# Kernel optimization log

Hardware: AMD Instinct MI355X
Metric: run time of the kernel (lower is better)

## Reference

```python
import jax, jax.numpy as jnp
import numpy as np

V, H, B, NS, SL, QL, AL = 100000, 256, 64, 40, 30, 20, 12
NUM_EPISODE = 3


def setup_inputs() -> dict:
    key = jax.random.key(0)
    ks = iter(jax.random.split(key, 48))
    def p(shape, scale=0.05):
        return jax.random.normal(next(ks), shape, jnp.float32) * scale
    d = {}
    d["c_p"] = jax.random.randint(next(ks), (B, NS, SL), 0, V, dtype=jnp.int32)
    d["c_mask"] = jnp.zeros((B, NS, SL), jnp.int32)
    d["q_p"] = jax.random.randint(next(ks), (B, QL), 0, V, dtype=jnp.int32)
    d["q_mask"] = jnp.zeros((B, QL), jnp.int32)
    d["a_I_p"] = jax.random.randint(next(ks), (B, AL), 0, V, dtype=jnp.int32)
    d["a_I_mask"] = jnp.zeros((B, AL), jnp.int32)
    d["a_II_p"] = jax.random.randint(next(ks), (B, AL), 0, V, dtype=jnp.int32)
    d["a_II_mask"] = jnp.zeros((B, AL), jnp.int32)
    d["embed"] = p((V, H)).at[0].set(0.0)  # padding_idx=0
    for name in ["ctx", "q", "ans", "attn", "mem"]:
        d[name + "_Wih"] = p((3 * H, H))
        d[name + "_Whh"] = p((3 * H, H))
        d[name + "_bih"] = p((3 * H,))
        d[name + "_bhh"] = p((3 * H,))
    d["gate_W1"] = p((H, 7 * H)); d["gate_b1"] = p((H,))
    d["gate_W2"] = p((1, H));     d["gate_b2"] = p((1,))
    d["out_W1"] = p((H, 3 * H)); d["out_b1"] = p((H,))
    d["out_W2"] = p((2, H));     d["out_b2"] = p((2,))
    return d


def _gru_step(h, gi_t, Whh, bhh):
    # PyTorch GRU cell math; gates ordered (r, z, n)
    gh = h @ Whh.T + bhh
    i_r, i_z, i_n = jnp.split(gi_t, 3, -1)
    h_r, h_z, h_n = jnp.split(gh, 3, -1)
    r = jax.nn.sigmoid(i_r + h_r)
    z = jax.nn.sigmoid(i_z + h_z)
    n = jnp.tanh(i_n + r * h_n)
    return (1.0 - z) * n + z * h


def _run_gru(x, Wih, Whh, bih, bhh):
    # x: [N, T, H] -> outputs [N, T, H], zero initial hidden
    gi = jnp.einsum('nth,gh->ntg', x, Wih) + bih  # precompute input projections
    h0 = jnp.zeros((x.shape[0], Whh.shape[1]), x.dtype)
    def step(h, g_t):
        h2 = _gru_step(h, g_t, Whh, bhh)
        return h2, h2
    _, outs = jax.lax.scan(step, h0, jnp.swapaxes(gi, 0, 1))
    return jnp.swapaxes(outs, 0, 1)


def _gather_last(outs, mask):
    # real_length = number of zeros in mask (0 marks a valid token)
    lengths = jnp.sum(mask == 0, axis=-1)
    idx = jnp.clip(lengths - 1, 0, outs.shape[1] - 1)
    return jnp.take_along_axis(outs, idx[:, None, None], axis=1)[:, 0]


def _forward(c_p, c_mask, q_p, q_mask, a_I_p, a_I_mask, a_II_p, a_II_mask,
             embed,
             ctx_Wih, ctx_Whh, ctx_bih, ctx_bhh,
             q_Wih, q_Whh, q_bih, q_bhh,
             ans_Wih, ans_Whh, ans_bih, ans_bhh,
             attn_Wih, attn_Whh, attn_bih, attn_bhh,
             mem_Wih, mem_Whh, mem_bih, mem_bhh,
             gate_W1, gate_b1, gate_W2, gate_b2,
             out_W1, out_b1, out_W2, out_b2):
    b, ns, sl = c_p.shape
    # Context encoding: all (batch, sentence) pairs through one batched GRU
    ce = embed[c_p.reshape(b * ns, sl)]                      # [B*NS, SL, H]
    c_out = _run_gru(ce, ctx_Wih, ctx_Whh, ctx_bih, ctx_bhh)
    enc_ctx = _gather_last(c_out, c_mask.reshape(b * ns, sl)).reshape(b, ns, -1)  # [B, NS, H]
    # Question / answers
    enc_q = _gather_last(_run_gru(embed[q_p], q_Wih, q_Whh, q_bih, q_bhh), q_mask)          # [B, H]
    enc_a1 = _gather_last(_run_gru(embed[a_I_p], ans_Wih, ans_Whh, ans_bih, ans_bhh), a_I_mask)
    enc_a2 = _gather_last(_run_gru(embed[a_II_p], ans_Wih, ans_Whh, ans_bih, ans_bhh), a_II_mask)
    # Episodic memory: gated attention GRU scan over context sentences
    ctx_t = jnp.swapaxes(enc_ctx, 0, 1)  # [NS, B, H]
    memory = enc_q
    for _ in range(NUM_EPISODE):
        mem_now = memory
        def step(h, ct):
            feat = jnp.concatenate([ct, mem_now, enc_q, ct * enc_q, ct * mem_now,
                                    jnp.abs(ct - enc_q), jnp.abs(ct - mem_now)], axis=1)  # [B, 7H]
            g = jax.nn.sigmoid(jnp.tanh(feat @ gate_W1.T + gate_b1) @ gate_W2.T + gate_b2)  # [B, 1]
            hc = _gru_step(h, ct @ attn_Wih.T + attn_bih, attn_Whh, attn_bhh)
            return g * hc + (1.0 - g) * h, None
        e, _ = jax.lax.scan(step, jnp.zeros_like(memory), ctx_t)
        memory = _gru_step(memory, e @ mem_Wih.T + mem_bih, mem_Whh, mem_bhh)
    final = jnp.concatenate([memory, enc_a1, enc_a2], axis=1)  # [B, 3H]
    logits = jnp.tanh(final @ out_W1.T + out_b1) @ out_W2.T + out_b2  # [B, 2]
    return jax.nn.softmax(logits, axis=-1)


def reference(c_p, c_mask, q_p, q_mask, a_I_p, a_I_mask, a_II_p, a_II_mask,
              embed,
              ctx_Wih, ctx_Whh, ctx_bih, ctx_bhh,
              q_Wih, q_Whh, q_bih, q_bhh,
              ans_Wih, ans_Whh, ans_bih, ans_bhh,
              attn_Wih, attn_Whh, attn_bih, attn_bhh,
              mem_Wih, mem_Whh, mem_bih, mem_bhh,
              gate_W1, gate_b1, gate_W2, gate_b2,
              out_W1, out_b1, out_W2, out_b2):
    return _forward(c_p, c_mask, q_p, q_mask, a_I_p, a_I_mask, a_II_p, a_II_mask,
                    embed,
                    ctx_Wih, ctx_Whh, ctx_bih, ctx_bhh,
                    q_Wih, q_Whh, q_bih, q_bhh,
                    ans_Wih, ans_Whh, ans_bih, ans_bhh,
                    attn_Wih, attn_Whh, attn_bih, attn_bhh,
                    mem_Wih, mem_Whh, mem_bih, mem_bhh,
                    gate_W1, gate_b1, gate_W2, gate_b2,
                    out_W1, out_b1, out_W2, out_b2)
```

## Files before the change

kernel.cpp:

```cpp
#include <hip/hip_runtime.h>

typedef unsigned short u16;
typedef __bf16 bf16x8 __attribute__((ext_vector_type(8)));
typedef float f32x4 __attribute__((ext_vector_type(4)));
typedef float f32x4v __attribute__((ext_vector_type(4)));
typedef unsigned int u32x2 __attribute__((ext_vector_type(2)));

#define NSENT 40
#define SLEN 30
#define QLEN 20
#define ALEN 12
#define SCTX 2560
#define SLOT 24
#define TP 12288

__device__ __forceinline__ float b2f(u16 u){ union{float f; unsigned i;} v; v.i = ((unsigned)u)<<16; return v.f; }
__device__ __forceinline__ u16 f2b(float f){ union{float f; unsigned u;} v; v.f=f; unsigned u=v.u; u += ((u>>16)&1u) + 0x7fffu; return (u16)(u>>16); }
__device__ __forceinline__ float sigm(float x){ return __builtin_amdgcn_rcpf(1.f + __expf(-x)); }
__device__ __forceinline__ float tanh_(float x){
  float a = fminf(fmaxf(2.f*x, -30.f), 30.f);
  float e = __expf(a);
  return 1.f - 2.f*__builtin_amdgcn_rcpf(e + 1.f);
}
__device__ __forceinline__ f32x4 mfma16(bf16x8 a, bf16x8 b, f32x4 c){
// ... 74 lines not shown
    *(u32x2*)&xb[row][f4*4] = pk;
  }
  const int w=tid>>6, lane=tid&63, c=lane&15, quad=lane>>4;
  __syncthreads();
  #pragma unroll
  for (int jj=0;jj<2;jj++){
    f32x4 acc[4][3];
    #pragma unroll
    for (int Mt=0;Mt<4;Mt++)
      #pragma unroll
      for (int g=0;g<3;g++) acc[Mt][g]=(f32x4){0.f,0.f,0.f,0.f};
    #pragma unroll
    for (int Kt=0;Kt<8;Kt++){
      bf16x8 a0=*(const bf16x8*)&xb[c][Kt*32+quad*8];
      bf16x8 a1=*(const bf16x8*)&xb[16+c][Kt*32+quad*8];
      bf16x8 a2=*(const bf16x8*)&xb[32+c][Kt*32+quad*8];
      bf16x8 a3=*(const bf16x8*)&xb[48+c][Kt*32+quad*8];
      #pragma unroll
      for (int g=0;g<3;g++){
        bf16x8 bfr=*(const bf16x8*)(W + (w*96+(jj*3+g)*16+c)*256 + Kt*32 + quad*8);
        acc[0][g]=mfma16(a0,bfr,acc[0][g]);
        acc[1][g]=mfma16(a1,bfr,acc[1][g]);
        acc[2][g]=mfma16(a2,bfr,acc[2][g]);
        acc[3][g]=mfma16(a3,bfr,acc[3][g]);
      }
    }
    float bv[3];
    #pragma unroll
    for (int g=0;g<3;g++) bv[g]=bias[w*96+(jj*3+g)*16+c];
    #pragma unroll
    for (int Mt=0;Mt<4;Mt++){
      int tp=Mt>>1, smh=Mt&1;
      unsigned d[6];
      #pragma unroll
      for (int k=0;k<6;k++){
        int s0=2*k, s1=2*k+1;
        int r0=s0/3, g0=s0%3, r1=s1/3, g1=s1%3;
        unsigned lo=f2b(acc[Mt][g0][r0]+bv[g0]);
        unsigned hi=f2b(acc[Mt][g1][r1]+bv[g1]);
        d[k]=lo|(hi<<16);
      }
      long block16 = (long)blk32*2 + smh;
      u16* dst = out + (block16*T + t0+tp)*TP + jj*6144 + (w*64+lane)*12;
      u32x2 s0v; s0v.x=d[0]; s0v.y=d[1];
      u32x2 s1v; s1v.x=d[2]; s1v.y=d[3];
      u32x2 s2v; s2v.x=d[4]; s2v.y=d[5];
      __builtin_nontemporal_store(s0v, (u32x2*)dst);
      __builtin_nontemporal_store(s1v, (u32x2*)(dst+4));
      __builtin_nontemporal_store(s2v, (u32x2*)(dst+8));
    }
  }
}

__global__ __launch_bounds__(512, 2) void k_enc_scan(
    const int* c_mask, const int* q_mask, const int* a1m, const int* a2m,
    const u16* cWhhP, const u16* qWhhP, const u16* aWhhP,
    const float* cBhh, const float* qBhh, const float* aBhh,
    const u16* gi_c, const u16* gi_q, const u16* gi_a1, const u16* gi_a2,
    u16* enc_hi, u16* enc_lo, float* enc_qf, float* enc_a1f, float* enc_a2f)
{
  __shared__ u16 hhi[16][264];
  __shared__ u16 hlo[16][264];
  __shared__ int idxs[16];
  int bid=blockIdx.x, tid=threadIdx.x;
  const int* msk; const u16* W; const float* bhh; const u16* gi; int T, seq0, mode;
  u16 *ohi=0, *olo=0; float* of=0;
  if (bid<160){ msk=c_mask; W=cWhhP; bhh=cBhh; gi=gi_c+(long)bid*SLEN*TP; T=SLEN; seq0=bid*16; mode=0; ohi=enc_hi; olo=enc_lo; }
  else if (bid<164){ int e=bid-160; msk=q_mask; W=qWhhP; bhh=qBhh; gi=gi_q+(long)e*QLEN*TP; T=QLEN; seq0=e*16; mode=1; of=enc_qf; }
  else if (bid<168){ int e=bid-164; msk=a1m; W=aWhhP; bhh=aBhh; gi=gi_a1+(long)e*ALEN*TP; T=ALEN; seq0=e*16; mode=1; of=enc_a1f; }
  else             { int e=bid-168; msk=a2m; W=aWhhP; bhh=aBhh; gi=gi_a2+(long)e*ALEN*TP; T=ALEN; seq0=e*16; mode=1; of=enc_a2f; }
  if (tid<16){
    int len=0; const int* mr=msk+(seq0+tid)*T;
    for (int t=0;t<T;t++) len += (mr[t]==0);
    int id=len-1; if(id<0)id=0; if(id>T-1)id=T-1; idxs[tid]=id;
  }
  for (int i=tid;i<16*264;i+=512){ ((u16*)hhi)[i]=0; ((u16*)hlo)[i]=0; }
  const int w=tid>>6, lane=tid&63, c=lane&15, quad=lane>>4;
  float biasv[6];
  #pragma unroll
  for (int nt=0;nt<6;nt++) biasv[nt]=bhh[w*96+nt*16+c];
  uint4 breg[48];
  #pragma unroll
  for (int nt=0;nt<6;nt++)
    #pragma unroll
    for (int Kt=0;Kt<8;Kt++)
      breg[nt*8+Kt] = *(const uint4*)(W + (w*96+nt*16+c)*256 + Kt*32 + quad*8);
  float hreg[8];
  #pragma unroll
  for (int i=0;i<8;i++) hreg[i]=0.f;
  const u16* gp = gi + (w*64+lane)*12;
  u32x2 pA0=*(const u32x2*)(gp),      pA1=*(const u32x2*)(gp+4),    pA2=*(const u32x2*)(gp+8);
  u32x2 pA3=*(const u32x2*)(gp+6144), pA4=*(const u32x2*)(gp+6148), pA5=*(const u32x2*)(gp+6152);
  __syncthreads();
  int idxr[4];
  #pragma unroll
  for (int r=0;r<4;r++) idxr[r]=idxs[quad*4+r];

  for (int t=0;t<T;t++){
    u32x2 pB0,pB1,pB2,pB3,pB4,pB5;
    bool pf=(t+1<T);
    if (pf){
      const u16* gn = gp + (long)(t+1)*TP;
      pB0=*(const u32x2*)(gn);      pB1=*(const u32x2*)(gn+4);    pB2=*(const u32x2*)(gn+8);
      pB3=*(const u32x2*)(gn+6144); pB4=*(const u32x2*)(gn+6148); pB5=*(const u32x2*)(gn+6152);
    }
    f32x4 acc[6];
    #pragma unroll
    for (int nt=0;nt<6;nt++) acc[nt]=(f32x4){0.f,0.f,0.f,0.f};
    #pragma unroll
    for (int Kt=0;Kt<8;Kt++){
      bf16x8 a=*(const bf16x8*)&hhi[c][Kt*32+quad*8];
      #pragma unroll
      for (int nt=0;nt<6;nt++) acc[nt]=mfma16(a,*(const bf16x8*)&breg[nt*8+Kt],acc[nt]);
    }
    #pragma unroll
    for (int Kt=0;Kt<8;Kt++){
      bf16x8 a=*(const bf16x8*)&hlo[c][Kt*32+quad*8];
      #pragma unroll
      for (int nt=0;nt<6;nt++) acc[nt]=mfma16(a,*(const bf16x8*)&breg[nt*8+Kt],acc[nt]);
    }
    unsigned pd[12];
    *(u32x2*)&pd[0]=pA0; *(u32x2*)&pd[2]=pA1; *(u32x2*)&pd[4]=pA2;
    *(u32x2*)&pd[6]=pA3; *(u32x2*)&pd[8]=pA4; *(u32x2*)&pd[10]=pA5;
    #pragma unroll
    for (int r=0;r<4;r++){
      int m=quad*4+r;
      #pragma unroll
      for (int jj=0;jj<2;jj++){
        int j=w*32+jj*16+c;
        int ib=r*3;
        float ir = b2f((u16)((pd[jj*6+(ib>>1)]     >> ((ib&1)*16)) & 0xffffu));
        float iz = b2f((u16)((pd[jj*6+((ib+1)>>1)] >> (((ib+1)&1)*16)) & 0xffffu));
        float in_= b2f((u16)((pd[jj*6+((ib+2)>>1)] >> (((ib+2)&1)*16)) & 0xffffu));
        float hr=acc[jj*3+0][r]+biasv[jj*3+0];
        float hz=acc[jj*3+1][r]+biasv[jj*3+1];
        float hn=acc[jj*3+2][r]+biasv[jj*3+2];
        float rr=sigm(ir+hr), zz=sigm(iz+hz), nn=tanh_(in_+rr*hn);
        float ho=hreg[r*2+jj];
        float hnew=(1.f-zz)*nn+zz*ho;
        hreg[r*2+jj]=hnew;
        u16 hi_=f2b(hnew); u16 lo_=f2b(hnew-b2f(hi_));
        hhi[m][j]=hi_; hlo[m][j]=lo_;
        if (t==idxr[r]){
          long o=(long)(seq0+m)*256+j;
          if (mode==0){ ohi[o]=hi_; olo[o]=lo_; }
          else of[o]=hnew;
        }
      }
    }
    __syncthreads();
    pA0=pB0; pA1=pB1; pA2=pB2; pA3=pB3; pA4=pB4; pA5=pB5;
  }
}

__global__ __launch_bounds__(512, 2) void k_gi(
    const u16* enc_hi, const u16* enc_lo, const u16* tWihP, const float* tBih,
    float* gi_attn, const float* enc_qf, float* mem_f)
{
  int bid=blockIdx.x, tid=threadIdx.x;
  if (bid==160){ for (int i=tid;i<64*256;i+=512) mem_f[i]=enc_qf[i]; return; }
  __shared__ u16 ahi[16][264];
  __shared__ u16 alo[16][264];
  int bblk=bid/40, s=bid-bblk*40, b0=bblk*16;
  {
    int row=tid>>5, ch=tid&31;
    long seq=(long)(b0+row)*NSENT + s;
    *(uint4*)((char*)&ahi[row][0]+ch*16) = *((const uint4*)(enc_hi+seq*256)+ch);
    *(uint4*)((char*)&alo[row][0]+ch*16) = *((const uint4*)(enc_lo+seq*256)+ch);
  }
  const int w=tid>>6, lane=tid&63, c=lane&15, quad=lane>>4;
  f32x4 acc[6];
  #pragma unroll
  for (int nt=0;nt<6;nt++) acc[nt]=(f32x4){0.f,0.f,0.f,0.f};
  __syncthreads();
  #pragma unroll
  for (int Kt=0;Kt<8;Kt++){
    bf16x8 a=*(const bf16x8*)&ahi[c][Kt*32+quad*8];
    #pragma unroll
    for (int nt=0;nt<6;nt++){
      bf16x8 bfr=*(const bf16x8*)(tWihP + (w*96+nt*16+c)*256 + Kt*32 + quad*8);
      acc[nt]=mfma16(a,bfr,acc[nt]);
    }
  }
  #pragma unroll
  for (int Kt=0;Kt<8;Kt++){
    bf16x8 a=*(const bf16x8*)&alo[c][Kt*32+quad*8];
    #pragma unroll
    for (int nt=0;nt<6;nt++){
      bf16x8 bfr=*(const bf16x8*)(tWihP + (w*96+nt*16+c)*256 + Kt*32 + quad*8);
      acc[nt]=mfma16(a,bfr,acc[nt]);
    }
  }
  float biasv[6];
  #pragma unroll
  for (int nt=0;nt<6;nt++) biasv[nt]=tBih[w*96+nt*16+c];
  float* dst = gi_attn + ((long)(bblk*40+s))*TP + (w*64+lane)*SLOT;
  #pragma unroll
  for (int d=0;d<6;d++){
    float4 v;
    #pragma unroll
    for (int e=0;e<4;e++){
      int idx=4*d+e;
      int r=idx/6, rem=idx%6, jj=rem/3, g=rem%3;
      ((float*)&v)[e]=acc[jj*3+g][r]+biasv[jj*3+g];
    }
    *(float4*)(dst+4*d)=v;
  }
}

__global__ __launch_bounds__(512, 1) void k_gatepre(
    const u16* enc_hi, const u16* enc_lo, const float* enc_qf,
    const u16* W1, const float* b1, float* partial)
{
  __shared__ float ctf[32][257];
  __shared__ float qvf[32][257];
  __shared__ u16 ab[32][264];
  int bid=blockIdx.x, tid=threadIdx.x, seq0=bid*32;
  #pragma unroll
  for (int p=0;p<16;p++){
    int i=p*512+tid; int row=i>>8, j=i&255;
    int grow=seq0+row; int b=grow/NSENT;
    ctf[row][j]=b2f(enc_hi[(long)grow*256+j])+b2f(enc_lo[(long)grow*256+j]);
    qvf[row][j]=enc_qf[b*256+j];
  }
  const int w=tid>>6, lane=tid&63, c=lane&15, quad=lane>>4;
  f32x4 acc[2][2];
  #pragma unroll
  for (int nt=0;nt<2;nt++){
    float bv=b1[(w*2+nt)*16+c];
    acc[0][nt]=(f32x4){bv,bv,bv,bv}; acc[1][nt]=acc[0][nt];
  }
  const int chl[4]={0,2,3,5};
  for (int ci=0; ci<4; ci++){
    int ch=chl[ci];
    __syncthreads();
    #pragma unroll
    for (int p=0;p<16;p++){
      int i=p*512+tid; int row=i>>8, j=i&255;
      float ct=ctf[row][j], qv=qvf[row][j];
      float v;
      if      (ch==0) v=ct;
      else if (ch==2) v=qv;
      else if (ch==3) v=ct*qv;
      else            v=fabsf(ct-qv);
      ab[row][j]=f2b(v);
    }
    __syncthreads();
    #pragma unroll
    for (int Kt=0;Kt<8;Kt++){
      bf16x8 a0=*(const bf16x8*)&ab[c][Kt*32+quad*8];
      bf16x8 a1=*(const bf16x8*)&ab[16+c][Kt*32+quad*8];
      #pragma unroll
      for (int nt=0;nt<2;nt++){
        int n=(w*2+nt)*16+c;
        bf16x8 bfr=*(const bf16x8*)(W1 + (long)n*1792 + ch*256 + Kt*32 + quad*8);
        acc[0][nt]=mfma16(a0,bfr,acc[0][nt]);
        acc[1][nt]=mfma16(a1,bfr,acc[1][nt]);
      }
    }
// ... 40 lines not shown
  for (int ci=0; ci<3; ci++){
    int ch=chl[ci];
    __syncthreads();
    #pragma unroll
    for (int p=0;p<16;p++){
      int i=p*512+tid; int row=i>>8, j=i&255;
      float ct=ctf[row][j], mv=mvf[row][j];
      float v;
      if      (ch==1) v=mv;
      else if (ch==4) v=ct*mv;
      else            v=fabsf(ct-mv);
      ab[row][j]=f2b(v);
    }
    __syncthreads();
    #pragma unroll
    for (int Kt=0;Kt<8;Kt++){
      bf16x8 a0=*(const bf16x8*)&ab[c][Kt*32+quad*8];
      bf16x8 a1=*(const bf16x8*)&ab[16+c][Kt*32+quad*8];
      #pragma unroll
      for (int nt=0;nt<2;nt++){
        int n=(w*2+nt)*16+c;
        bf16x8 bfr=*(const bf16x8*)(W1 + (long)n*1792 + ch*256 + Kt*32 + quad*8);
        acc[0][nt]=mfma16(a0,bfr,acc[0][nt]);
        acc[1][nt]=mfma16(a1,bfr,acc[1][nt]);
      }
    }
  }
  float pm[8];
  #pragma unroll
  for (int i=0;i<8;i++){
    int Mt=i>>2, r=i&3;
    float s=0.f;
    #pragma unroll
    for (int nt=0;nt<2;nt++) s += tanh_(acc[Mt][nt][r])*w2v[nt];
    pm[i]=s;
  }
  #pragma unroll
  for (int off=1;off<16;off<<=1)
    #pragma unroll
    for (int i=0;i<8;i++) pm[i]+=__shfl_xor(pm[i],off,64);
  if (c==0){
    #pragma unroll
    for (int i=0;i<8;i++){ int m=(i>>2)*16+quad*4+(i&3); pl[m][w]=pm[i]; }
  }
  __syncthreads();
  if (tid<32){
    float s=b2v[0];
    #pragma unroll
    for (int ww=0;ww<8;ww++) s+=pl[tid][ww];
    g[seq0+tid]=sigm(s);
  }
}

__global__ __launch_bounds__(512, 2) void k_scan(
    const u16* tWhhP, const float* tBhh,
    const float* gi_attn, const float* g,
    float* mem_f, const u16* mWihP, const u16* mWhhP,
    const float* mBih, const float* mBhh)
{
  __shared__ u16 hb[16][264];
  __shared__ u16 mhi[16][264];
  __shared__ u16 mlo[16][264];
  __shared__ float memfl[16][256];
  __shared__ float gl[16][40];
  int bid=blockIdx.x, tid=threadIdx.x, b0=bid*16;
  const int w=tid>>6, lane=tid&63, c=lane&15, quad=lane>>4;
  for (int i=tid;i<16*264;i+=512){ ((u16*)hb)[i]=0; }
  for (int i=tid;i<4096;i+=512){
    int m=i>>8, j=i&255;
    float v=mem_f[(b0+m)*256+j]; memfl[m][j]=v;
    u16 hi_=f2b(v); mhi[m][j]=hi_; mlo[m][j]=f2b(v-b2f(hi_));
  }
  for (int i=tid;i<640;i+=512){ int m=i/40, s=i-m*40; gl[m][s]=g[(b0+m)*40+s]; }
  float biasv[6];
  #pragma unroll
  for (int nt=0;nt<6;nt++) biasv[nt]=tBhh[w*96+nt*16+c];
  uint4 breg[48];
  #pragma unroll
  for (int nt=0;nt<6;nt++)
    #pragma unroll
    for (int Kt=0;Kt<8;Kt++)
      breg[nt*8+Kt] = *(const uint4*)(tWhhP + (w*96+nt*16+c)*256 + Kt*32 + quad*8);
  float hreg[8];
  #pragma unroll
  for (int i=0;i<8;i++) hreg[i]=0.f;
  const float* gp = gi_attn + ((long)bid*NSENT)*TP + (w*64+lane)*SLOT;
  float4 pA[6];
  #pragma unroll
  for (int d=0;d<6;d++) pA[d]=*(const float4*)(gp+4*d);
  __syncthreads();

  for (int s=0;s<NSENT;s++){
    float4 pB[6];
    bool pf=(s+1<NSENT);
    if (pf){
      const float* gn = gp + (long)(s+1)*TP;
      #pragma unroll
      for (int d=0;d<6;d++) pB[d]=*(const float4*)(gn+4*d);
    }
    f32x4 acc[6];
    #pragma unroll
    for (int nt=0;nt<6;nt++) acc[nt]=(f32x4){0.f,0.f,0.f,0.f};
    #pragma unroll
    for (int Kt=0;Kt<8;Kt++){
      bf16x8 a=*(const bf16x8*)&hb[c][Kt*32+quad*8];
      #pragma unroll
      for (int nt=0;nt<6;nt++) acc[nt]=mfma16(a,*(const bf16x8*)&breg[nt*8+Kt],acc[nt]);
    }
    const float* pf32 = (const float*)&pA[0];
    #pragma unroll
    for (int r=0;r<4;r++){
      int m=quad*4+r;
      float gv = gl[m][s];
      #pragma unroll
      for (int jj=0;jj<2;jj++){
        int j=w*32+jj*16+c;
        int ib=(r*2+jj)*3;
        float ir=pf32[ib], iz=pf32[ib+1], in_=pf32[ib+2];
        float hr=acc[jj*3+0][r]+biasv[jj*3+0];
        float hz=acc[jj*3+1][r]+biasv[jj*3+1];
        float hn=acc[jj*3+2][r]+biasv[jj*3+2];
        float rr=sigm(ir+hr), zz=sigm(iz+hz), nn=tanh_(in_+rr*hn);
        float ho=hreg[r*2+jj];
        float hc=(1.f-zz)*nn+zz*ho;
        float hnew=gv*hc+(1.f-gv)*ho;
        hreg[r*2+jj]=hnew;
        hb[m][j]=f2b(hnew);
      }
    }
    __syncthreads();
    #pragma unroll
    for (int d=0;d<6;d++) pA[d]=pB[d];
  }
  f32x4 ai[6], ah[6];
  #pragma unroll
  for (int nt=0;nt<6;nt++){ ai[nt]=(f32x4){0.f,0.f,0.f,0.f}; ah[nt]=ai[nt]; }
  #pragma unroll
  for (int Kt=0;Kt<8;Kt++){
    bf16x8 a=*(const bf16x8*)&hb[c][Kt*32+quad*8];
    #pragma unroll
    for (int nt=0;nt<6;nt++){
      bf16x8 bfr=*(const bf16x8*)(mWihP + (w*96+nt*16+c)*256 + Kt*32 + quad*8);
      ai[nt]=mfma16(a,bfr,ai[nt]);
    }
  }
  #pragma unroll
  for (int Kt=0;Kt<8;Kt++){
    bf16x8 a=*(const bf16x8*)&mhi[c][Kt*32+quad*8];
    #pragma unroll
    for (int nt=0;nt<6;nt++){
      bf16x8 bfr=*(const bf16x8*)(mWhhP + (w*96+nt*16+c)*256 + Kt*32 + quad*8);
      ah[nt]=mfma16(a,bfr,ah[nt]);
    }
  }
  #pragma unroll
  for (int Kt=0;Kt<8;Kt++){
    bf16x8 a=*(const bf16x8*)&mlo[c][Kt*32+quad*8];
    #pragma unroll
    for (int nt=0;nt<6;nt++){
      bf16x8 bfr=*(const bf16x8*)(mWhhP + (w*96+nt*16+c)*256 + Kt*32 + quad*8);
      ah[nt]=mfma16(a,bfr,ah[nt]);
    }
  }
  float bih6[6], bhh6[6];
  #pragma unroll
  for (int nt=0;nt<6;nt++){ bih6[nt]=mBih[w*96+nt*16+c]; bhh6[nt]=mBhh[w*96+nt*16+c]; }
  #pragma unroll
  for (int r=0;r<4;r++){
    int m=quad*4+r;
    #pragma unroll
    for (int jj=0;jj<2;jj++){
      int j=w*32+jj*16+c;
      float ir=ai[jj*3+0][r]+bih6[jj*3+0];
      float iz=ai[jj*3+1][r]+bih6[jj*3+1];
      float in_=ai[jj*3+2][r]+bih6[jj*3+2];
      float hr=ah[jj*3+0][r]+bhh6[jj*3+0];
      float hz=ah[jj*3+1][r]+bhh6[jj*3+1];
      float hn=ah[jj*3+2][r]+bhh6[jj*3+2];
      float rr=sigm(ir+hr), zz=sigm(iz+hz), nn=tanh_(in_+rr*hn);
      float mo=memfl[m][j];
      mem_f[(b0+m)*256+j]=(1.f-zz)*nn+zz*mo;
    }
  }
}

__global__ void k_final(const float* mem_f, const float* a1f, const float* a2f,
    const float* W1o, const float* b1o, const float* W2o, const float* b2o, float* outp)
{
  __shared__ float af[768];
  __shared__ float tl[256];
  __shared__ float lg[2];
  int b=blockIdx.x, tid=threadIdx.x;
  af[tid]     = mem_f[b*256+tid];
  af[256+tid] = a1f[b*256+tid];
  af[512+tid] = a2f[b*256+tid];
  __syncthreads();
  float s=b1o[tid];
  const float* wr=W1o + (long)tid*768;
  for (int k=0;k<768;k++) s += af[k]*wr[k];
  tl[tid]=tanh_(s);
  __syncthreads();
  if (tid<2){
    float l=b2o[tid];
    const float* w2=W2o + tid*256;
    for (int k=0;k<256;k++) l += tl[k]*w2[k];
    lg[tid]=l;
  }
  __syncthreads();
  if (tid==0){
    float m=fmaxf(lg[0],lg[1]);
    float e0=__expf(lg[0]-m), e1=__expf(lg[1]-m);
    float inv=1.f/(e0+e1);
    outp[b*2]=e0*inv; outp[b*2+1]=e1*inv;
  }
}

extern "C" void kernel_launch(void* const* d_in, const int* in_sizes, int n_in,
                              void* d_out, int out_size, void* d_ws, size_t ws_size,
                              hipStream_t stream) {
  const int* c_p   = (const int*)d_in[0];
  const int* c_m   = (const int*)d_in[1];
  const int* q_p   = (const int*)d_in[2];
  const int* q_m   = (const int*)d_in[3];
  const int* a1p   = (const int*)d_in[4];
  const int* a1m   = (const int*)d_in[5];
  const int* a2p   = (const int*)d_in[6];
  const int* a2m   = (const int*)d_in[7];
  const float* embed = (const float*)d_in[8];
  const float* cWih=(const float*)d_in[9],  *cWhh=(const float*)d_in[10], *cbih=(const float*)d_in[11], *cbhh=(const float*)d_in[12];
  const float* qWih=(const float*)d_in[13], *qWhh=(const float*)d_in[14], *qbih=(const float*)d_in[15], *qbhh=(const float*)d_in[16];
  const float* aWih=(const float*)d_in[17], *aWhh=(const float*)d_in[18], *abih=(const float*)d_in[19], *abhh=(const float*)d_in[20];
  const float* tWih=(const float*)d_in[21], *tWhh=(const float*)d_in[22], *tbih=(const float*)d_in[23], *tbhh=(const float*)d_in[24];
  const float* mWih=(const float*)d_in[25], *mWhh=(const float*)d_in[26], *mbih=(const float*)d_in[27], *mbhh=(const float*)d_in[28];
  const float* gW1=(const float*)d_in[29], *gb1=(const float*)d_in[30], *gW2=(const float*)d_in[31], *gb2=(const float*)d_in[32];
  const float* oW1=(const float*)d_in[33], *ob1=(const float*)d_in[34], *oW2=(const float*)d_in[35], *ob2=(const float*)d_in[36];

  char* ws = (char*)d_ws;
  size_t off = 0;
  u16* P[10];
  for (int i=0;i<10;i++){ P[i]=(u16*)(ws+off); off+=393216; }
  u16* PgW1 =(u16*)(ws+off); off+=917504;
  float* B[10];
  for (int i=0;i<10;i++){ B[i]=(float*)(ws+off); off+=3072; }
  u16* gi_c =(u16*)(ws+off); off+=(size_t)160*SLEN*TP*2;
  u16* gi_q =(u16*)(ws+off); off+=(size_t)4*QLEN*TP*2;
  u16* gi_a1=(u16*)(ws+off); off+=(size_t)4*ALEN*TP*2;
  u16* gi_a2=(u16*)(ws+off); off+=(size_t)4*ALEN*TP*2;
  u16* enc_hi=(u16*)(ws+off); off+=(size_t)SCTX*256*2;
  u16* enc_lo=(u16*)(ws+off); off+=(size_t)SCTX*256*2;
  float* enc_qf =(float*)(ws+off); off+=64*256*4;
  float* enc_a1f=(float*)(ws+off); off+=64*256*4;
  float* enc_a2f=(float*)(ws+off); off+=64*256*4;
  float* mem_f  =(float*)(ws+off); off+=64*256*4;
  float* gi_attn=(float*)(ws+off); off+=(size_t)160*TP*4;
  float* partial=(float*)(ws+off); off+=(size_t)SCTX*256*4;
  float* gbuf   =(float*)(ws+off); off+=SCTX*4;

  k_prep<<<4751, 512, 0, stream>>>(cWih,cWhh,qWih,qWhh,aWih,aWhh,tWih,tWhh,mWih,mWhh,gW1,
      cbih,cbhh,qbih,qbhh,abih,abhh,tbih,tbhh,mbih,mbhh,
      P[0],P[1],P[2],P[3],P[4],P[5],P[6],P[7],P[8],P[9], PgW1,
      B[0],B[1],B[2],B[3],B[4],B[5],B[6],B[7],B[8],B[9]);

  k_xproj<<<1244, 512, 0, stream>>>(c_p,q_p,a1p,a2p, embed,
      P[0],P[2],P[4], B[0],B[2],B[4], gi_c,gi_q,gi_a1,gi_a2);

  k_enc_scan<<<172, 512, 0, stream>>>(c_m,q_m,a1m,a2m,
      P[1],P[3],P[5], B[1],B[3],B[5], gi_c,gi_q,gi_a1,gi_a2,
      enc_hi,enc_lo, enc_qf,enc_a1f,enc_a2f);

  k_gi<<<161, 512, 0, stream>>>(enc_hi,enc_lo, P[6], B[6], gi_attn, enc_qf, mem_f);

  k_gatepre<<<80, 512, 0, stream>>>(enc_hi,enc_lo, enc_qf, PgW1, gb1, partial);

  for (int ep=0; ep<3; ep++){
    k_gate<<<80, 512, 0, stream>>>(enc_hi,enc_lo, mem_f, partial, PgW1, gW2, gb2, gbuf);
    k_scan<<<4, 512, 0, stream>>>(P[7], B[7], gi_attn, gbuf, mem_f, P[8], P[9], B[8], B[9]);
  }

  k_final<<<64, 256, 0, stream>>>(mem_f, enc_a1f, enc_a2f, oW1, ob1, oW2, ob2, (float*)d_out);
}
```

Measured before the change: 893.6 us.

## Double threads per block in recurrent scan kernels, halving per-wave hidden-unit work

The encoder scan and attention scan kernels move from 512 to 1024 threads per block. Each of the 16 waves now owns 16 hidden units (3 gate tiles) instead of 32, which halves the MFMA chain and gate math per wave on every serial timestep. The gi_attn output layout in k_gi is changed to match the new per-wave slicing. The cost is one block per CU and more waves taking part in each per-step barrier. The shorter serial chain per timestep is meant to cut latency on these latency-bound recurrences.

```diff
diff --git a/kernel.cpp b/kernel.cpp
--- a/kernel.cpp
+++ b/kernel.cpp
@@ -150,7 +150,7 @@
   }
 }
 
-__global__ __launch_bounds__(512, 2) void k_enc_scan(
+__global__ __launch_bounds__(1024, 1) void k_enc_scan(
     const int* c_mask, const int* q_mask, const int* a1m, const int* a2m,
     const u16* cWhhP, const u16* qWhhP, const u16* aWhhP,
     const float* cBhh, const float* qBhh, const float* aBhh,
@@ -172,82 +172,76 @@
     for (int t=0;t<T;t++) len += (mr[t]==0);
     int id=len-1; if(id<0)id=0; if(id>T-1)id=T-1; idxs[tid]=id;
   }
-  for (int i=tid;i<16*264;i+=512){ ((u16*)hhi)[i]=0; ((u16*)hlo)[i]=0; }
+  for (int i=tid;i<16*264;i+=1024){ ((u16*)hhi)[i]=0; ((u16*)hlo)[i]=0; }
   const int w=tid>>6, lane=tid&63, c=lane&15, quad=lane>>4;
-  float biasv[6];
-  #pragma unroll
-  for (int nt=0;nt<6;nt++) biasv[nt]=bhh[w*96+nt*16+c];
-  uint4 breg[48];
-  #pragma unroll
-  for (int nt=0;nt<6;nt++)
+  const int j=w*16+c;
+  float biasv[3];
+  #pragma unroll
+  for (int g=0;g<3;g++) biasv[g]=bhh[w*48+g*16+c];
+  uint4 breg[24];
+  #pragma unroll
+  for (int g=0;g<3;g++)
     #pragma unroll
     for (int Kt=0;Kt<8;Kt++)
-      breg[nt*8+Kt] = *(const uint4*)(W + (w*96+nt*16+c)*256 + Kt*32 + quad*8);
-  float hreg[8];
-  #pragma unroll
-  for (int i=0;i<8;i++) hreg[i]=0.f;
-  const u16* gp = gi + (w*64+lane)*12;
-  u32x2 pA0=*(const u32x2*)(gp),      pA1=*(const u32x2*)(gp+4),    pA2=*(const u32x2*)(gp+8);
-  u32x2 pA3=*(const u32x2*)(gp+6144), pA4=*(const u32x2*)(gp+6148), pA5=*(const u32x2*)(gp+6152);
+      breg[g*8+Kt] = *(const uint4*)(W + (w*48+g*16+c)*256 + Kt*32 + quad*8);
+  float hreg[4];
+  #pragma unroll
+  for (int i=0;i<4;i++) hreg[i]=0.f;
+  const u16* gp = gi + (w&1)*6144 + ((w>>1)*64+lane)*12;
+  u32x2 pA0=*(const u32x2*)(gp), pA1=*(const u32x2*)(gp+4), pA2=*(const u32x2*)(gp+8);
   __syncthreads();
   int idxr[4];
   #pragma unroll
   for (int r=0;r<4;r++) idxr[r]=idxs[quad*4+r];
 
   for (int t=0;t<T;t++){
-    u32x2 pB0,pB1,pB2,pB3,pB4,pB5;
+    u32x2 pB0,pB1,pB2;
     bool pf=(t+1<T);
     if (pf){
       const u16* gn = gp + (long)(t+1)*TP;
-      pB0=*(const u32x2*)(gn);      pB1=*(const u32x2*)(gn+4);    pB2=*(const u32x2*)(gn+8);
-      pB3=*(const u32x2*)(gn+6144); pB4=*(const u32x2*)(gn+6148); pB5=*(const u32x2*)(gn+6152);
-    }
-    f32x4 acc[6];
-    #pragma unroll
-    for (int nt=0;nt<6;nt++) acc[nt]=(f32x4){0.f,0.f,0.f,0.f};
+      pB0=*(const u32x2*)(gn); pB1=*(const u32x2*)(gn+4); pB2=*(const u32x2*)(gn+8);
+    }
+    f32x4 acc[3];
+    #pragma unroll
+    for (int g=0;g<3;g++) acc[g]=(f32x4){0.f,0.f,0.f,0.f};
     #pragma unroll
     for (int Kt=0;Kt<8;Kt++){
       bf16x8 a=*(const bf16x8*)&hhi[c][Kt*32+quad*8];
       #pragma unroll
-      for (int nt=0;nt<6;nt++) acc[nt]=mfma16(a,*(const bf16x8*)&breg[nt*8+Kt],acc[nt]);
+      for (int g=0;g<3;g++) acc[g]=mfma16(a,*(const bf16x8*)&breg[g*8+Kt],acc[g]);
     }
     #pragma unroll
     for (int Kt=0;Kt<8;Kt++){
       bf16x8 a=*(const bf16x8*)&hlo[c][Kt*32+quad*8];
       #pragma unroll
-      for (int nt=0;nt<6;nt++) acc[nt]=mfma16(a,*(const bf16x8*)&breg[nt*8+Kt],acc[nt]);
-    }
-    unsigned pd[12];
+      for (int g=0;g<3;g++) acc[g]=mfma16(a,*(const bf16x8*)&breg[g*8+Kt],acc[g]);
+    }
+    unsigned pd[6];
     *(u32x2*)&pd[0]=pA0; *(u32x2*)&pd[2]=pA1; *(u32x2*)&pd[4]=pA2;
-    *(u32x2*)&pd[6]=pA3; *(u32x2*)&pd[8]=pA4; *(u32x2*)&pd[10]=pA5;
     #pragma unroll
     for (int r=0;r<4;r++){
       int m=quad*4+r;
-      #pragma unroll
-      for (int jj=0;jj<2;jj++){
-        int j=w*32+jj*16+c;
-        int ib=r*3;
-        float ir = b2f((u16)((pd[jj*6+(ib>>1)]     >> ((ib&1)*16)) & 0xffffu));
-        float iz = b2f((u16)((pd[jj*6+((ib+1)>>1)] >> (((ib+1)&1)*16)) & 0xffffu));
-        float in_= b2f((u16)((pd[jj*6+((ib+2)>>1)] >> (((ib+2)&1)*16)) & 0xffffu));
-        float hr=acc[jj*3+0][r]+biasv[jj*3+0];
-        float hz=acc[jj*3+1][r]+biasv[jj*3+1];
-        float hn=acc[jj*3+2][r]+biasv[jj*3+2];
-        float rr=sigm(ir+hr), zz=sigm(iz+hz), nn=tanh_(in_+rr*hn);
-        float ho=hreg[r*2+jj];
-        float hnew=(1.f-zz)*nn+zz*ho;
-        hreg[r*2+jj]=hnew;
-        u16 hi_=f2b(hnew); u16 lo_=f2b(hnew-b2f(hi_));
-        hhi[m][j]=hi_; hlo[m][j]=lo_;
-        if (t==idxr[r]){
-          long o=(long)(seq0+m)*256+j;
-          if (mode==0){ ohi[o]=hi_; olo[o]=lo_; }
-          else of[o]=hnew;
-        }
+      int ib=r*3;
+      float ir = b2f((u16)((pd[ib>>1]     >> ((ib&1)*16)) & 0xffffu));
+      float iz = b2f((u16)((pd[(ib+1)>>1] >> (((ib+1)&1)*16)) & 0xffffu));
+      float in_= b2f((u16)((pd[(ib+2)>>1] >> (((ib+2)&1)*16)) & 0xffffu));
+      float hr=acc[0][r]+biasv[0];
+      float hz=acc[1][r]+biasv[1];
+      float hn=acc[2][r]+biasv[2];
+      float rr=sigm(ir+hr), zz=sigm(iz+hz), nn=tanh_(in_+rr*hn);
+      float ho=hreg[r];
+      float hnew=(1.f-zz)*nn+zz*ho;
+      hreg[r]=hnew;
+      u16 hi_=f2b(hnew); u16 lo_=f2b(hnew-b2f(hi_));
+      hhi[m][j]=hi_; hlo[m][j]=lo_;
+      if (t==idxr[r]){
+        long o=(long)(seq0+m)*256+j;
+        if (mode==0){ ohi[o]=hi_; olo[o]=lo_; }
+        else of[o]=hnew;
       }
     }
     __syncthreads();
-    pA0=pB0; pA1=pB1; pA2=pB2; pA3=pB3; pA4=pB4; pA5=pB5;
+    pA0=pB0; pA1=pB1; pA2=pB2;
   }
 }
 
@@ -292,17 +286,20 @@
   float biasv[6];
   #pragma unroll
   for (int nt=0;nt<6;nt++) biasv[nt]=tBih[w*96+nt*16+c];
-  float* dst = gi_attn + ((long)(bblk*40+s))*TP + (w*64+lane)*SLOT;
-  #pragma unroll
-  for (int d=0;d<6;d++){
-    float4 v;
-    #pragma unroll
-    for (int e=0;e<4;e++){
-      int idx=4*d+e;
-      int r=idx/6, rem=idx%6, jj=rem/3, g=rem%3;
-      ((float*)&v)[e]=acc[jj*3+g][r]+biasv[jj*3+g];
-    }
-    *(float4*)(dst+4*d)=v;
+  #pragma unroll
+  for (int jj=0;jj<2;jj++){
+    float* dst = gi_attn + ((long)(bblk*40+s))*TP + jj*6144 + (w*64+lane)*12;
+    #pragma unroll
+    for (int d=0;d<3;d++){
+      float4 v;
+      #pragma unroll
+      for (int e=0;e<4;e++){
+        int idx=4*d+e;
+        int r=idx/3, g=idx%3;
+        ((float*)&v)[e]=acc[jj*3+g][r]+biasv[jj*3+g];
+      }
+      *(float4*)(dst+4*d)=v;
+    }
   }
 }
 
@@ -449,7 +446,7 @@
   }
 }
 
-__global__ __launch_bounds__(512, 2) void k_scan(
+__global__ __launch_bounds__(1024, 1) void k_scan(
     const u16* tWhhP, const float* tBhh,
     const float* gi_attn, const float* g,
     float* mem_f, const u16* mWihP, const u16* mWhhP,
@@ -462,122 +459,115 @@
   __shared__ float gl[16][40];
   int bid=blockIdx.x, tid=threadIdx.x, b0=bid*16;
   const int w=tid>>6, lane=tid&63, c=lane&15, quad=lane>>4;
-  for (int i=tid;i<16*264;i+=512){ ((u16*)hb)[i]=0; }
-  for (int i=tid;i<4096;i+=512){
-    int m=i>>8, j=i&255;
-    float v=mem_f[(b0+m)*256+j]; memfl[m][j]=v;
-    u16 hi_=f2b(v); mhi[m][j]=hi_; mlo[m][j]=f2b(v-b2f(hi_));
-  }
-  for (int i=tid;i<640;i+=512){ int m=i/40, s=i-m*40; gl[m][s]=g[(b0+m)*40+s]; }
-  float biasv[6];
-  #pragma unroll
-  for (int nt=0;nt<6;nt++) biasv[nt]=tBhh[w*96+nt*16+c];
-  uint4 breg[48];
-  #pragma unroll
-  for (int nt=0;nt<6;nt++)
+  const int j=w*16+c;
+  for (int i=tid;i<16*264;i+=1024){ ((u16*)hb)[i]=0; }
+  for (int i=tid;i<4096;i+=1024){
+    int m=i>>8, jx=i&255;
+    float v=mem_f[(b0+m)*256+jx]; memfl[m][jx]=v;
+    u16 hi_=f2b(v); mhi[m][jx]=hi_; mlo[m][jx]=f2b(v-b2f(hi_));
+  }
+  for (int i=tid;i<640;i+=1024){ int m=i/40, s=i-m*40; gl[m][s]=g[(b0+m)*40+s]; }
+  float biasv[3];
+  #pragma unroll
+  for (int gg=0;gg<3;gg++) biasv[gg]=tBhh[w*48+gg*16+c];
+  uint4 breg[24];
+  #pragma unroll
+  for (int gg=0;gg<3;gg++)
     #pragma unroll
     for (int Kt=0;Kt<8;Kt++)
-      breg[nt*8+Kt] = *(const uint4*)(tWhhP + (w*96+nt*16+c)*256 + Kt*32 + quad*8);
-  float hreg[8];
-  #pragma unroll
-  for (int i=0;i<8;i++) hreg[i]=0.f;
-  const float* gp = gi_attn + ((long)bid*NSENT)*TP + (w*64+lane)*SLOT;
-  float4 pA[6];
-  #pragma unroll
-  for (int d=0;d<6;d++) pA[d]=*(const float4*)(gp+4*d);
+      breg[gg*8+Kt] = *(const uint4*)(tWhhP + (w*48+gg*16+c)*256 + Kt*32 + quad*8);
+  float hreg[4];
+  #pragma unroll
+  for (int i=0;i<4;i++) hreg[i]=0.f;
+  const float* gp = gi_attn + ((long)bid*NSENT)*TP + (w&1)*6144 + ((w>>1)*64+lane)*12;
+  float4 pA[3];
+  #pragma unroll
+  for (int d=0;d<3;d++) pA[d]=*(const float4*)(gp+4*d);
   __syncthreads();
 
   for (int s=0;s<NSENT;s++){
-    float4 pB[6];
+    float4 pB[3];
     bool pf=(s+1<NSENT);
     if (pf){
       const float* gn = gp + (long)(s+1)*TP;
       #pragma unroll
-      for (int d=0;d<6;d++) pB[d]=*(const float4*)(gn+4*d);
-    }
-    f32x4 acc[6];
-    #pragma unroll
-    for (int nt=0;nt<6;nt++) acc[nt]=(f32x4){0.f,0.f,0.f,0.f};
+      for (int d=0;d<3;d++) pB[d]=*(const float4*)(gn+4*d);
+    }
+    f32x4 acc[3];
+    #pragma unroll
+    for (int gg=0;gg<3;gg++) acc[gg]=(f32x4){0.f,0.f,0.f,0.f};
     #pragma unroll
     for (int Kt=0;Kt<8;Kt++){
       bf16x8 a=*(const bf16x8*)&hb[c][Kt*32+quad*8];
       #pragma unroll
-      for (int nt=0;nt<6;nt++) acc[nt]=mfma16(a,*(const bf16x8*)&breg[nt*8+Kt],acc[nt]);
+      for (int gg=0;gg<3;gg++) acc[gg]=mfma16(a,*(const bf16x8*)&breg[gg*8+Kt],acc[gg]);
     }
     const float* pf32 = (const float*)&pA[0];
     #pragma unroll
     for (int r=0;r<4;r++){
       int m=quad*4+r;
       float gv = gl[m][s];
-      #pragma unroll
-      for (int jj=0;jj<2;jj++){
-        int j=w*32+jj*16+c;
-        int ib=(r*2+jj)*3;
-        float ir=pf32[ib], iz=pf32[ib+1], in_=pf32[ib+2];
-        float hr=acc[jj*3+0][r]+biasv[jj*3+0];
-        float hz=acc[jj*3+1][r]+biasv[jj*3+1];
-        float hn=acc[jj*3+2][r]+biasv[jj*3+2];
-        float rr=sigm(ir+hr), zz=sigm(iz+hz), nn=tanh_(in_+rr*hn);
-        float ho=hreg[r*2+jj];
-        float hc=(1.f-zz)*nn+zz*ho;
-        float hnew=gv*hc+(1.f-gv)*ho;
-        hreg[r*2+jj]=hnew;
-        hb[m][j]=f2b(hnew);
-      }
+      int ib=r*3;
+      float ir=pf32[ib], iz=pf32[ib+1], in_=pf32[ib+2];
+      float hr=acc[0][r]+biasv[0];
+      float hz=acc[1][r]+biasv[1];
+      float hn=acc[2][r]+biasv[2];
+      float rr=sigm(ir+hr), zz=sigm(iz+hz), nn=tanh_(in_+rr*hn);
+      float ho=hreg[r];
+      float hc=(1.f-zz)*nn+zz*ho;
+      float hnew=gv*hc+(1.f-gv)*ho;
+      hreg[r]=hnew;
+      hb[m][j]=f2b(hnew);
     }
     __syncthreads();
     #pragma unroll
-    for (int d=0;d<6;d++) pA[d]=pB[d];
-  }
-  f32x4 ai[6], ah[6];
-  #pragma unroll
-  for (int nt=0;nt<6;nt++){ ai[nt]=(f32x4){0.f,0.f,0.f,0.f}; ah[nt]=ai[nt]; }
+    for (int d=0;d<3;d++) pA[d]=pB[d];
+  }
+  f32x4 ai[3], ah[3];
+  #pragma unroll
+  for (int gg=0;gg<3;gg++){ ai[gg]=(f32x4){0.f,0.f,0.f,0.f}; ah[gg]=ai[gg]; }
   #pragma unroll
   for (int Kt=0;Kt<8;Kt++){
     bf16x8 a=*(const bf16x8*)&hb[c][Kt*32+quad*8];
     #pragma unroll
-    for (int nt=0;nt<6;nt++){
-      bf16x8 bfr=*(const bf16x8*)(mWihP + (w*96+nt*16+c)*256 + Kt*32 + quad*8);
-      ai[nt]=mfma16(a,bfr,ai[nt]);
+    for (int gg=0;gg<3;gg++){
+      bf16x8 bfr=*(const bf16x8*)(mWihP + (w*48+gg*16+c)*256 + Kt*32 + quad*8);
+      ai[gg]=mfma16(a,bfr,ai[gg]);
     }
   }
   #pragma unroll
   for (int Kt=0;Kt<8;Kt++){
     bf16x8 a=*(const bf16x8*)&mhi[c][Kt*32+quad*8];
     #pragma unroll
-    for (int nt=0;nt<6;nt++){
-      bf16x8 bfr=*(const bf16x8*)(mWhhP + (w*96+nt*16+c)*256 + Kt*32 + quad*8);
-      ah[nt]=mfma16(a,bfr,ah[nt]);
+    for (int gg=0;gg<3;gg++){
+      bf16x8 bfr=*(const bf16x8*)(mWhhP + (w*48+gg*16+c)*256 + Kt*32 + quad*8);
+      ah[gg]=mfma16(a,bfr,ah[gg]);
     }
   }
   #pragma unroll
   for (int Kt=0;Kt<8;Kt++){
     bf16x8 a=*(const bf16x8*)&mlo[c][Kt*32+quad*8];
     #pragma unroll
-    for (int nt=0;nt<6;nt++){
-      bf16x8 bfr=*(const bf16x8*)(mWhhP + (w*96+nt*16+c)*256 + Kt*32 + quad*8);
-      ah[nt]=mfma16(a,bfr,ah[nt]);
-    }
-  }
-  float bih6[6], bhh6[6];
-  #pragma unroll
-  for (int nt=0;nt<6;nt++){ bih6[nt]=mBih[w*96+nt*16+c]; bhh6[nt]=mBhh[w*96+nt*16+c]; }
+    for (int gg=0;gg<3;gg++){
+      bf16x8 bfr=*(const bf16x8*)(mWhhP + (w*48+gg*16+c)*256 + Kt*32 + quad*8);
+      ah[gg]=mfma16(a,bfr,ah[gg]);
+    }
+  }
+  float bih3[3], bhh3[3];
+  #pragma unroll
+  for (int gg=0;gg<3;gg++){ bih3[gg]=mBih[w*48+gg*16+c]; bhh3[gg]=mBhh[w*48+gg*16+c]; }
   #pragma unroll
   for (int r=0;r<4;r++){
     int m=quad*4+r;
-    #pragma unroll
-    for (int jj=0;jj<2;jj++){
-      int j=w*32+jj*16+c;
-      float ir=ai[jj*3+0][r]+bih6[jj*3+0];
-      float iz=ai[jj*3+1][r]+bih6[jj*3+1];
-      float in_=ai[jj*3+2][r]+bih6[jj*3+2];
-      float hr=ah[jj*3+0][r]+bhh6[jj*3+0];
-      float hz=ah[jj*3+1][r]+bhh6[jj*3+1];
-      float hn=ah[jj*3+2][r]+bhh6[jj*3+2];
-      float rr=sigm(ir+hr), zz=sigm(iz+hz), nn=tanh_(in_+rr*hn);
-      float mo=memfl[m][j];
-      mem_f[(b0+m)*256+j]=(1.f-zz)*nn+zz*mo;
-    }
+    float ir=ai[0][r]+bih3[0];
+    float iz=ai[1][r]+bih3[1];
+    float in_=ai[2][r]+bih3[2];
+    float hr=ah[0][r]+bhh3[0];
+    float hz=ah[1][r]+bhh3[1];
+    float hn=ah[2][r]+bhh3[2];
+    float rr=sigm(ir+hr), zz=sigm(iz+hz), nn=tanh_(in_+rr*hn);
+    float mo=memfl[m][j];
+    mem_f[(b0+m)*256+j]=(1.f-zz)*nn+zz*mo;
   }
 }
 
@@ -661,7 +651,7 @@
   k_xproj<<<1244, 512, 0, stream>>>(c_p,q_p,a1p,a2p, embed,
       P[0],P[2],P[4], B[0],B[2],B[4], gi_c,gi_q,gi_a1,gi_a2);
 
-  k_enc_scan<<<172, 512, 0, stream>>>(c_m,q_m,a1m,a2m,
+  k_enc_scan<<<172, 1024, 0, stream>>>(c_m,q_m,a1m,a2m,
       P[1],P[3],P[5], B[1],B[3],B[5], gi_c,gi_q,gi_a1,gi_a2,
       enc_hi,enc_lo, enc_qf,enc_a1f,enc_a2f);
 
@@ -671,7 +661,7 @@
 
   for (int ep=0; ep<3; ep++){
     k_gate<<<80, 512, 0, stream>>>(enc_hi,enc_lo, mem_f, partial, PgW1, gW2, gb2, gbuf);
-    k_scan<<<4, 512, 0, stream>>>(P[7], B[7], gi_attn, gbuf, mem_f, P[8], P[9], B[8], B[9]);
+    k_scan<<<4, 1024, 0, stream>>>(P[7], B[7], gi_attn, gbuf, mem_f, P[8], P[9], B[8], B[9]);
   }
 
   k_final<<<64, 256, 0, stream>>>(mem_f, enc_a1f, enc_a2f, oW1, ob1, oW2, ob2, (float*)d_out);
```

After: 1.295 ms. 1.45x slower.

## Process two 16-sequence groups per encoder-scan block, reading Whh from global

Applied to the files above, without the earlier changes.

Each encoder GRU scan block now handles 32 sequences (two 16-row halves) instead of 16, halving the grid from 172 to 86 blocks. Recurrent weights are no longer held in 48 uint4 registers; they are reloaded from global or cache inside each time step and shared across both halves. The intent is to raise MFMA work per weight fetch and free registers, while the hi/lo split MFMAs are interleaved. In exchange, fewer blocks run (86 on a 256-CU part) and per-step global weight loads add latency to the sequential critical path.

```diff
diff --git a/kernel.cpp b/kernel.cpp
--- a/kernel.cpp
+++ b/kernel.cpp
@@ -150,104 +150,125 @@
   }
 }
 
-__global__ __launch_bounds__(512, 2) void k_enc_scan(
+__global__ __launch_bounds__(512, 1) void k_enc_scan(
     const int* c_mask, const int* q_mask, const int* a1m, const int* a2m,
     const u16* cWhhP, const u16* qWhhP, const u16* aWhhP,
     const float* cBhh, const float* qBhh, const float* aBhh,
     const u16* gi_c, const u16* gi_q, const u16* gi_a1, const u16* gi_a2,
     u16* enc_hi, u16* enc_lo, float* enc_qf, float* enc_a1f, float* enc_a2f)
 {
-  __shared__ u16 hhi[16][264];
-  __shared__ u16 hlo[16][264];
-  __shared__ int idxs[16];
+  __shared__ u16 hhi[32][264];
+  __shared__ u16 hlo[32][264];
+  __shared__ int idxs[32];
   int bid=blockIdx.x, tid=threadIdx.x;
   const int* msk; const u16* W; const float* bhh; const u16* gi; int T, seq0, mode;
   u16 *ohi=0, *olo=0; float* of=0;
-  if (bid<160){ msk=c_mask; W=cWhhP; bhh=cBhh; gi=gi_c+(long)bid*SLEN*TP; T=SLEN; seq0=bid*16; mode=0; ohi=enc_hi; olo=enc_lo; }
-  else if (bid<164){ int e=bid-160; msk=q_mask; W=qWhhP; bhh=qBhh; gi=gi_q+(long)e*QLEN*TP; T=QLEN; seq0=e*16; mode=1; of=enc_qf; }
-  else if (bid<168){ int e=bid-164; msk=a1m; W=aWhhP; bhh=aBhh; gi=gi_a1+(long)e*ALEN*TP; T=ALEN; seq0=e*16; mode=1; of=enc_a1f; }
-  else             { int e=bid-168; msk=a2m; W=aWhhP; bhh=aBhh; gi=gi_a2+(long)e*ALEN*TP; T=ALEN; seq0=e*16; mode=1; of=enc_a2f; }
-  if (tid<16){
+  if (bid<80){ msk=c_mask; W=cWhhP; bhh=cBhh; gi=gi_c+(long)bid*2*SLEN*TP; T=SLEN; seq0=bid*32; mode=0; ohi=enc_hi; olo=enc_lo; }
+  else if (bid<82){ int e=bid-80; msk=q_mask; W=qWhhP; bhh=qBhh; gi=gi_q+(long)e*2*QLEN*TP; T=QLEN; seq0=e*32; mode=1; of=enc_qf; }
+  else if (bid<84){ int e=bid-82; msk=a1m; W=aWhhP; bhh=aBhh; gi=gi_a1+(long)e*2*ALEN*TP; T=ALEN; seq0=e*32; mode=1; of=enc_a1f; }
+  else            { int e=bid-84; msk=a2m; W=aWhhP; bhh=aBhh; gi=gi_a2+(long)e*2*ALEN*TP; T=ALEN; seq0=e*32; mode=1; of=enc_a2f; }
+  if (tid<32){
     int len=0; const int* mr=msk+(seq0+tid)*T;
     for (int t=0;t<T;t++) len += (mr[t]==0);
     int id=len-1; if(id<0)id=0; if(id>T-1)id=T-1; idxs[tid]=id;
   }
-  for (int i=tid;i<16*264;i+=512){ ((u16*)hhi)[i]=0; ((u16*)hlo)[i]=0; }
+  for (int i=tid;i<32*264;i+=512){ ((u16*)hhi)[i]=0; ((u16*)hlo)[i]=0; }
   const int w=tid>>6, lane=tid&63, c=lane&15, quad=lane>>4;
   float biasv[6];
   #pragma unroll
   for (int nt=0;nt<6;nt++) biasv[nt]=bhh[w*96+nt*16+c];
-  uint4 breg[48];
-  #pragma unroll
-  for (int nt=0;nt<6;nt++)
-    #pragma unroll
-    for (int Kt=0;Kt<8;Kt++)
-      breg[nt*8+Kt] = *(const uint4*)(W + (w*96+nt*16+c)*256 + Kt*32 + quad*8);
-  float hreg[8];
-  #pragma unroll
-  for (int i=0;i<8;i++) hreg[i]=0.f;
-  const u16* gp = gi + (w*64+lane)*12;
-  u32x2 pA0=*(const u32x2*)(gp),      pA1=*(const u32x2*)(gp+4),    pA2=*(const u32x2*)(gp+8);
-  u32x2 pA3=*(const u32x2*)(gp+6144), pA4=*(const u32x2*)(gp+6148), pA5=*(const u32x2*)(gp+6152);
-  __syncthreads();
-  int idxr[4];
-  #pragma unroll
-  for (int r=0;r<4;r++) idxr[r]=idxs[quad*4+r];
+  float hreg[16];
+  #pragma unroll
+  for (int i=0;i<16;i++) hreg[i]=0.f;
+  const u16* gpl = gi + (w*64+lane)*12;
+  const u16* Wb  = W + (w*96+c)*256 + quad*8;
+  u32x2 pA[12];
+  #pragma unroll
+  for (int hf=0;hf<2;hf++)
+    #pragma unroll
+    for (int jj=0;jj<2;jj++){
+      const u16* p = gpl + ((long)hf*T)*TP + jj*6144;
+      pA[(hf*2+jj)*3+0]=*(const u32x2*)(p);
+      pA[(hf*2+jj)*3+1]=*(const u32x2*)(p+4);
+      pA[(hf*2+jj)*3+2]=*(const u32x2*)(p+8);
+    }
+  __syncthreads();
+  int idxr[8];
+  #pragma unroll
+  for (int hf=0;hf<2;hf++)
+    #pragma unroll
+    for (int r=0;r<4;r++) idxr[hf*4+r]=idxs[hf*16+quad*4+r];
 
   for (int t=0;t<T;t++){
-    u32x2 pB0,pB1,pB2,pB3,pB4,pB5;
+    u32x2 pB[12];
     bool pf=(t+1<T);
     if (pf){
-      const u16* gn = gp + (long)(t+1)*TP;
-      pB0=*(const u32x2*)(gn);      pB1=*(const u32x2*)(gn+4);    pB2=*(const u32x2*)(gn+8);
-      pB3=*(const u32x2*)(gn+6144); pB4=*(const u32x2*)(gn+6148); pB5=*(const u32x2*)(gn+6152);
-    }
-    f32x4 acc[6];
-    #pragma unroll
-    for (int nt=0;nt<6;nt++) acc[nt]=(f32x4){0.f,0.f,0.f,0.f};
+      #pragma unroll
+      for (int hf=0;hf<2;hf++)
+        #pragma unroll
+        for (int jj=0;jj<2;jj++){
+          const u16* p = gpl + ((long)hf*T + t+1)*TP + jj*6144;
+          pB[(hf*2+jj)*3+0]=*(const u32x2*)(p);
+          pB[(hf*2+jj)*3+1]=*(const u32x2*)(p+4);
+          pB[(hf*2+jj)*3+2]=*(const u32x2*)(p+8);
+        }
+    }
+    f32x4 acc[2][6];
+    #pragma unroll
+    for (int hf=0;hf<2;hf++)
+      #pragma unroll
+      for (int nt=0;nt<6;nt++) acc[hf][nt]=(f32x4){0.f,0.f,0.f,0.f};
     #pragma unroll
     for (int Kt=0;Kt<8;Kt++){
-      bf16x8 a=*(const bf16x8*)&hhi[c][Kt*32+quad*8];
-      #pragma unroll
-      for (int nt=0;nt<6;nt++) acc[nt]=mfma16(a,*(const bf16x8*)&breg[nt*8+Kt],acc[nt]);
-    }
-    #pragma unroll
-    for (int Kt=0;Kt<8;Kt++){
-      bf16x8 a=*(const bf16x8*)&hlo[c][Kt*32+quad*8];
-      #pragma unroll
-      for (int nt=0;nt<6;nt++) acc[nt]=mfma16(a,*(const bf16x8*)&breg[nt*8+Kt],acc[nt]);
-    }
-    unsigned pd[12];
-    *(u32x2*)&pd[0]=pA0; *(u32x2*)&pd[2]=pA1; *(u32x2*)&pd[4]=pA2;
-    *(u32x2*)&pd[6]=pA3; *(u32x2*)&pd[8]=pA4; *(u32x2*)&pd[10]=pA5;
-    #pragma unroll
-    for (int r=0;r<4;r++){
-      int m=quad*4+r;
+      bf16x8 ah0=*(const bf16x8*)&hhi[c][Kt*32+quad*8];
+      bf16x8 ah1=*(const bf16x8*)&hhi[16+c][Kt*32+quad*8];
+      bf16x8 al0=*(const bf16x8*)&hlo[c][Kt*32+quad*8];
+      bf16x8 al1=*(const bf16x8*)&hlo[16+c][Kt*32+quad*8];
+      #pragma unroll
+      for (int nt=0;nt<6;nt++){
+        bf16x8 bfr=*(const bf16x8*)(Wb + nt*4096 + Kt*32);
+        acc[0][nt]=mfma16(ah0,bfr,acc[0][nt]);
+        acc[0][nt]=mfma16(al0,bfr,acc[0][nt]);
+        acc[1][nt]=mfma16(ah1,bfr,acc[1][nt]);
+        acc[1][nt]=mfma16(al1,bfr,acc[1][nt]);
+      }
+    }
+    #pragma unroll
+    for (int hf=0;hf<2;hf++){
       #pragma unroll
       for (int jj=0;jj<2;jj++){
-        int j=w*32+jj*16+c;
-        int ib=r*3;
-        float ir = b2f((u16)((pd[jj*6+(ib>>1)]     >> ((ib&1)*16)) & 0xffffu));
-        float iz = b2f((u16)((pd[jj*6+((ib+1)>>1)] >> (((ib+1)&1)*16)) & 0xffffu));
-        float in_= b2f((u16)((pd[jj*6+((ib+2)>>1)] >> (((ib+2)&1)*16)) & 0xffffu));
-        float hr=acc[jj*3+0][r]+biasv[jj*3+0];
-        float hz=acc[jj*3+1][r]+biasv[jj*3+1];
-        float hn=acc[jj*3+2][r]+biasv[jj*3+2];
-        float rr=sigm(ir+hr), zz=sigm(iz+hz), nn=tanh_(in_+rr*hn);
-        float ho=hreg[r*2+jj];
-        float hnew=(1.f-zz)*nn+zz*ho;
-        hreg[r*2+jj]=hnew;
-        u16 hi_=f2b(hnew); u16 lo_=f2b(hnew-b2f(hi_));
-        hhi[m][j]=hi_; hlo[m][j]=lo_;
-        if (t==idxr[r]){
-          long o=(long)(seq0+m)*256+j;
-          if (mode==0){ ohi[o]=hi_; olo[o]=lo_; }
-          else of[o]=hnew;
+        unsigned pd[6];
+        *(u32x2*)&pd[0]=pA[(hf*2+jj)*3+0];
+        *(u32x2*)&pd[2]=pA[(hf*2+jj)*3+1];
+        *(u32x2*)&pd[4]=pA[(hf*2+jj)*3+2];
+        #pragma unroll
+        for (int r=0;r<4;r++){
+          int ib=r*3;
+          float ir = b2f((u16)((pd[ib>>1]     >> ((ib&1)*16)) & 0xffffu));
+          float iz = b2f((u16)((pd[(ib+1)>>1] >> (((ib+1)&1)*16)) & 0xffffu));
+          float in_= b2f((u16)((pd[(ib+2)>>1] >> (((ib+2)&1)*16)) & 0xffffu));
+          float hr=acc[hf][jj*3+0][r]+biasv[jj*3+0];
+          float hz=acc[hf][jj*3+1][r]+biasv[jj*3+1];
+          float hn=acc[hf][jj*3+2][r]+biasv[jj*3+2];
+          float rr=sigm(ir+hr), zz=sigm(iz+hz), nn=tanh_(in_+rr*hn);
+          int hx=hf*8+r*2+jj;
+          float ho=hreg[hx];
+          float hnew=(1.f-zz)*nn+zz*ho;
+          hreg[hx]=hnew;
+          u16 hi_=f2b(hnew); u16 lo_=f2b(hnew-b2f(hi_));
+          int m=hf*16+quad*4+r, j=w*32+jj*16+c;
+          hhi[m][j]=hi_; hlo[m][j]=lo_;
+          if (t==idxr[hf*4+r]){
+            long o=(long)(seq0+m)*256+j;
+            if (mode==0){ ohi[o]=hi_; olo[o]=lo_; }
+            else of[o]=hnew;
+          }
         }
       }
     }
     __syncthreads();
-    pA0=pB0; pA1=pB1; pA2=pB2; pA3=pB3; pA4=pB4; pA5=pB5;
+    #pragma unroll
+    for (int i=0;i<12;i++) pA[i]=pB[i];
   }
 }
 
@@ -661,7 +682,7 @@
   k_xproj<<<1244, 512, 0, stream>>>(c_p,q_p,a1p,a2p, embed,
       P[0],P[2],P[4], B[0],B[2],B[4], gi_c,gi_q,gi_a1,gi_a2);
 
-  k_enc_scan<<<172, 512, 0, stream>>>(c_m,q_m,a1m,a2m,
+  k_enc_scan<<<86, 512, 0, stream>>>(c_m,q_m,a1m,a2m,
       P[1],P[3],P[5], B[1],B[3],B[5], gi_c,gi_q,gi_a1,gi_a2,
       enc_hi,enc_lo, enc_qf,enc_a1f,enc_a2f);
 
```

Result: slower. 1.226 ms (+37.2%).
